# Kernel optimization log

Measured on AMD Instinct MI355X. Metric: run time of the kernel, lower is better.

Reference implementation:

```python
import jax, jax.numpy as jnp
import numpy as np

PATCH = 3  # match_patch_size

def _to_patches(fm, nph, npw):
    # fm: [1, C, H, W] -> [nph*npw, C*PATCH*PATCH] non-overlapping 3x3 patches
    C = fm.shape[1]
    x = fm[0, :, :nph * PATCH, :npw * PATCH].reshape(C, nph, PATCH, npw, PATCH)
    x = x.transpose(1, 3, 0, 2, 4)  # [nph, npw, C, p, p]
    return x.reshape(nph * npw, C * PATCH * PATCH)

def _from_patches(p, nph, npw, C):
    # [nph*npw, C*p*p] -> [1, C, nph*p, npw*p]
    x = p.reshape(nph, npw, C, PATCH, PATCH).transpose(2, 0, 3, 1, 4)
    return x.reshape(1, C, nph * PATCH, npw * PATCH)

def setup_inputs() -> dict:
    key = jax.random.key(0)
    k1, k2, k3 = jax.random.split(key, 3)
    C, H, W = 512, 252, 252
    style_fm = jax.random.normal(k1, (1, C, H, W), dtype=jnp.float32)
    img_fm = jax.random.normal(k2, (1, C, H, W), dtype=jnp.float32)
    mask = jax.random.uniform(k3, (1, 1, H, W), dtype=jnp.float32)
    return {"style_fm": style_fm, "img_fm": img_fm, "mask": mask}

def reference(style_fm, img_fm, mask):
    B, C, H, W = style_fm.shape  # B == 1
    nph, npw = H // PATCH, W // PATCH
    # Patch match: each img patch is a conv kernel applied to style_fm with
    # stride=PATCH -> score positions == non-overlapping style patch grid.
    img_p = _to_patches(img_fm, nph, npw)      # [P, D]
    sty_p = _to_patches(style_fm, nph, npw)    # [Q, D]
    scores = img_p @ sty_p.T                   # [P, Q] cross-correlation
    idx = jnp.argmax(scores, axis=1)           # best style patch per img patch
    matched = sty_p[idx]                       # [P, D] gather
    matched_fm = _from_patches(matched, nph, npw, C)
    style_matched = style_fm.at[:, :, :nph * PATCH, :npw * PATCH].set(matched_fm)
    # Mask (expanded as in capture_content), then Gram / sum(expanded mask)
    masked = style_matched * mask
    mask_sum = jnp.sum(jnp.broadcast_to(mask, style_matched.shape))
    gram = jnp.einsum('bchw,bdhw->bcd', masked, masked) / mask_sum  # [1, C, C]
    return gram
```

## Files before the change

### kernel.cpp

```cpp
#include <hip/hip_runtime.h>
#include <stdint.h>

typedef _Float16 f16;
typedef _Float16 f16x8 __attribute__((ext_vector_type(8)));
typedef float f32x4 __attribute__((ext_vector_type(4)));

#define NCH   512
#define IMH   252
#define IMW   252
#define HWSZ  (IMH*IMW)
#define NP    84
#define PN    (NP*NP)
#define PPAD  7168
#define DD    (NCH*9)
#define KK2   (PPAD*9)
#define KSPLIT 48
#define KCH   (KK2/KSPLIT)
#define MARGIN 1.0f

#define AS1(p) ((const __attribute__((address_space(1))) void*)(p))
#define AS3(p) ((__attribute__((address_space(3))) void*)(p))

__global__ void k_init(f16* __restrict__ I, f16* __restrict__ S,
                       int* cnt, float* msum) {
  unsigned t = blockIdx.x * blockDim.x + threadIdx.x;
  if (t == 0) { *cnt = 0; *msum = 0.0f; }
  const unsigned padN = (PPAD - PN) * DD;
  for (unsigned i = t; i < padN; i += gridDim.x * blockDim.x) {
    I[(size_t)PN * DD + i] = (f16)0.0f;
    S[(size_t)PN * DD + i] = (f16)0.0f;
  }
}

__global__ void k_masksum(const float* __restrict__ mask, float* msum) {
  __shared__ float red[256];
  float s = 0.f;
  for (unsigned i = blockIdx.x * 256 + threadIdx.x; i < HWSZ; i += gridDim.x * 256)
    s += mask[i];
  red[threadIdx.x] = s; __syncthreads();
  for (int st = 128; st > 0; st >>= 1) {
    if ((int)threadIdx.x < st) red[threadIdx.x] += red[threadIdx.x + st];
    __syncthreads();
  }
  if (threadIdx.x == 0) atomicAdd(msum, red[0]);
}

__global__ void k_pack(const float* __restrict__ fm, f16* __restrict__ out) {
  const unsigned total8 = PN * DD / 8;
  for (unsigned e8 = blockIdx.x * blockDim.x + threadIdx.x; e8 < total8;
       e8 += gridDim.x * blockDim.x) {
    const unsigned base = e8 * 8;
    const unsigned p = base / DD;
    const unsigned d0 = base - p * DD;
    const unsigned py = (p / NP) * 3, px = (p % NP) * 3;
    f16x8 v;
#pragma unroll
    for (int k = 0; k < 8; ++k) {
      unsigned d = d0 + k;
      unsigned c = d / 9, j = d - c * 9;
      v[k] = (f16)fm[(size_t)c * HWSZ + (py + j / 3) * IMW + px + j % 3];
    }
    *(f16x8*)(out + base) = v;
  }
}

__global__ __launch_bounds__(256, 3)
void k_gemm(const f16* __restrict__ A, const f16* __restrict__ B,
            f16* __restrict__ out) {
  __shared__ f16 As[128][32];
  __shared__ f16 Bs[128][32];
  const int tid = threadIdx.x;
  const int w = tid >> 6, l = tid & 63;
  const int nwg = (PPAD / 128) * (PPAD / 128);
  int bid = blockIdx.x;
  bid = (bid & 7) * (nwg >> 3) + (bid >> 3);
  const int bx = bid % (PPAD / 128), by = bid / (PPAD / 128);
  const size_t row0 = (size_t)by * 128, col0 = (size_t)bx * 128;
  const int wr = w >> 1, wc = w & 1;
  f32x4 acc[4][4] = {};
  const int sr = w * 32 + (l >> 2);
  const int skb = (l & 3) * 8;
  const f16* ga = A + (row0 + sr) * DD + skb;
  const f16* gb = B + (col0 + sr) * DD + skb;
  f16* lA0 = &As[w * 32][0];  f16* lA1 = &As[w * 32 + 16][0];
  f16* lB0 = &Bs[w * 32][0];  f16* lB1 = &Bs[w * 32 + 16][0];
  const int fr = l & 15, kb = (l >> 4) * 8;
  for (int k0 = 0; k0 < DD; k0 += 32) {
    __syncthreads();
    __builtin_amdgcn_global_load_lds(AS1(ga),           AS3(lA0), 16, 0, 0);
    __builtin_amdgcn_global_load_lds(AS1(ga + 16 * DD), AS3(lA1), 16, 0, 0);
    __builtin_amdgcn_global_load_lds(AS1(gb),           AS3(lB0), 16, 0, 0);
    __builtin_amdgcn_global_load_lds(AS1(gb + 16 * DD), AS3(lB1), 16, 0, 0);
    ga += 32; gb += 32;
    asm volatile("s_waitcnt vmcnt(0)" ::: "memory");
    __syncthreads();
    f16x8 af[4], bf[4];
#pragma unroll
    for (int i = 0; i < 4; ++i) af[i] = *(const f16x8*)&As[wr * 64 + i * 16 + fr][kb];
#pragma unroll
    for (int j = 0; j < 4; ++j) bf[j] = *(const f16x8*)&Bs[wc * 64 + j * 16 + fr][kb];
#pragma unroll
    for (int i = 0; i < 4; ++i)
#pragma unroll
      for (int j = 0; j < 4; ++j)
        acc[i][j] = __builtin_amdgcn_mfma_f32_16x16x32_f16(af[i], bf[j], acc[i][j], 0, 0, 0);
  }
  const int fq = l >> 4;
  const size_t orow = row0 + wr * 64, ocol = col0 + wc * 64;
#pragma unroll
  for (int i = 0; i < 4; ++i)
#pragma unroll
    for (int j = 0; j < 4; ++j)
#pragma unroll
      for (int r = 0; r < 4; ++r)
        out[(orow + i * 16 + fq * 4 + r) * PPAD + (ocol + j * 16 + fr)] =
            (f16)acc[i][j][r];
}

__global__ void k_top2(const f16* __restrict__ sc, int* __restrict__ idx,
                       float* __restrict__ max1v, int* __restrict__ amb, int* cnt) {
  const int p = blockIdx.x;
  const f16x8* row8 = (const f16x8*)(sc + (size_t)p * PPAD);
  float m1 = -1e30f, m2 = -1e30f; int i1 = 0;
  for (int v = threadIdx.x; v < PN / 8; v += 256) {
    f16x8 x = row8[v];
#pragma unroll
    for (int k = 0; k < 8; ++k) {
      float val = (float)x[k];
      if (val > m1) { m2 = m1; m1 = val; i1 = v * 8 + k; }
      else if (val > m2) m2 = val;
    }
  }
  __shared__ float sm1[256], sm2[256]; __shared__ int si1[256];
  const int t = threadIdx.x;
  sm1[t] = m1; sm2[t] = m2; si1[t] = i1; __syncthreads();
  for (int st = 128; st > 0; st >>= 1) {
    if (t < st) {
      float am1 = sm1[t], am2 = sm2[t]; int ai1 = si1[t];
      float bm1 = sm1[t + st], bm2 = sm2[t + st]; int bi1 = si1[t + st];
      if (bm1 > am1 || (bm1 == am1 && bi1 < ai1)) {
        sm1[t] = bm1; si1[t] = bi1; sm2[t] = fmaxf(am1, bm2);
      } else {
        sm2[t] = fmaxf(bm1, am2);
      }
    }
    __syncthreads();
  }
  if (t == 0) {
    idx[p] = si1[0]; max1v[p] = sm1[0];
    if (sm2[0] > sm1[0] - MARGIN) { int a = atomicAdd(cnt, 1); amb[a] = p; }
  }
}

__global__ void k_rescore(const float* __restrict__ img, const float* __restrict__ sty,
                          const f16* __restrict__ sc, const float* __restrict__ max1v,
                          const int* __restrict__ amb, const int* __restrict__ cnt,
                          int* __restrict__ idx) {
  __shared__ float red[256];
  __shared__ unsigned long long ball[4];
  const int t = threadIdx.x;
  const int n = *cnt;
  for (int r = blockIdx.x; r < n; r += gridDim.x) {
    const int p = amb[r];
    const float thr = max1v[p] - MARGIN;
    const f16* row = sc + (size_t)p * PPAD;
    const int py = (p / NP) * 3, px = (p % NP) * 3;
    float best = -1e30f; int bq = 0x7fffffff;
    for (int base = 0; base < PN; base += 256) {
      const int q = base + t;
      const bool is_cand = (q < PN) && ((float)row[q] >= thr);
      unsigned long long m = __ballot(is_cand);
      if ((t & 63) == 0) ball[t >> 6] = m;
      __syncthreads();
      for (int wv = 0; wv < 4; ++wv) {
        unsigned long long mm = ball[wv];
        while (mm) {
          const int b = __ffsll(mm) - 1; mm &= mm - 1;
          const int q2 = base + wv * 64 + b;
          const int qy = (q2 / NP) * 3, qx = (q2 % NP) * 3;
          float s = 0.f;
          for (int d = t; d < DD; d += 256) {
            int c = d / 9, j = d - c * 9, dy = j / 3, dx = j - dy * 3;
            s += img[(size_t)c * HWSZ + (py + dy) * IMW + (px + dx)] *
                 sty[(size_t)c * HWSZ + (qy + dy) * IMW + (qx + dx)];
          }
          red[t] = s; __syncthreads();
          for (int st = 128; st > 0; st >>= 1) {
            if (t < st) red[t] += red[t + st];
            __syncthreads();
          }
          const float tot = red[0];
          __syncthreads();
          if (tot > best || (tot == best && q2 < bq)) { best = tot; bq = q2; }
        }
      }
      __syncthreads();
    }
    if (t == 0) idx[p] = bq;
    __syncthreads();
  }
}

__global__ void k_masked(const f16* __restrict__ S, const int* __restrict__ idx,
                         const float* __restrict__ mask, f16* __restrict__ M) {
  const int p = blockIdx.x;
  if (p >= PN) {
    for (int e = threadIdx.x; e < NCH * 9; e += 256) {
      int c = e / 9, j = e - c * 9;
      M[(size_t)c * KK2 + p * 9 + j] = (f16)0.0f;
    }
    return;
  }
  __shared__ float mk[9];
  __shared__ int qs;
  if (threadIdx.x == 0) qs = idx[p];
  if (threadIdx.x < 9) {
    int j = threadIdx.x;
    mk[j] = mask[((p / NP) * 3 + j / 3) * IMW + (p % NP) * 3 + j % 3];
  }
  __syncthreads();
  const f16* srow = S + (size_t)qs * DD;
  for (int e = threadIdx.x; e < NCH * 9; e += 256) {
    int c = e / 9, j = e - c * 9;
    M[(size_t)c * KK2 + p * 9 + j] = (f16)((float)srow[e] * mk[j]);
  }
}

__global__ __launch_bounds__(256, 3)
void k_gram(const f16* __restrict__ M, float* __restrict__ part) {
  __shared__ f16 As[128][32];
  __shared__ f16 Bs[128][32];
  const int tid = threadIdx.x;
  const int w = tid >> 6, l = tid & 63;
  const int tile = blockIdx.x & 15, chunk = blockIdx.x >> 4;
  const int bx = tile & 3, by = tile >> 2;
  const size_t row0 = (size_t)by * 128, col0 = (size_t)bx * 128;
  const int wr = w >> 1, wc = w & 1;
  f32x4 acc[4][4] = {};
  const int sr = w * 32 + (l >> 2);
  const int skb = (l & 3) * 8;
  const int kbeg = chunk * KCH;
  const f16* ga = M + (row0 + sr) * KK2 + kbeg + skb;
  const f16* gb = M + (col0 + sr) * KK2 + kbeg + skb;
  f16* lA0 = &As[w * 32][0];  f16* lA1 = &As[w * 32 + 16][0];
  f16* lB0 = &Bs[w * 32][0];  f16* lB1 = &Bs[w * 32 + 16][0];
  const int fr = l & 15, kb = (l >> 4) * 8;
  for (int k0 = 0; k0 < KCH; k0 += 32) {
    __syncthreads();
    __builtin_amdgcn_global_load_lds(AS1(ga),            AS3(lA0), 16, 0, 0);
    __builtin_amdgcn_global_load_lds(AS1(ga + 16 * KK2), AS3(lA1), 16, 0, 0);
    __builtin_amdgcn_global_load_lds(AS1(gb),            AS3(lB0), 16, 0, 0);
    __builtin_amdgcn_global_load_lds(AS1(gb + 16 * KK2), AS3(lB1), 16, 0, 0);
    ga += 32; gb += 32;
    asm volatile("s_waitcnt vmcnt(0)" ::: "memory");
    __syncthreads();
    f16x8 af[4], bf[4];
#pragma unroll
    for (int i = 0; i < 4; ++i) af[i] = *(const f16x8*)&As[wr * 64 + i * 16 + fr][kb];
#pragma unroll
    for (int j = 0; j < 4; ++j) bf[j] = *(const f16x8*)&Bs[wc * 64 + j * 16 + fr][kb];
#pragma unroll
    for (int i = 0; i < 4; ++i)
#pragma unroll
      for (int j = 0; j < 4; ++j)
        acc[i][j] = __builtin_amdgcn_mfma_f32_16x16x32_f16(af[i], bf[j], acc[i][j], 0, 0, 0);
  }
  const int fq = l >> 4;
  const size_t orow = row0 + wr * 64, ocol = col0 + wc * 64;
  float* pout = part + (size_t)chunk * (NCH * NCH);
#pragma unroll
  for (int i = 0; i < 4; ++i)
#pragma unroll
    for (int j = 0; j < 4; ++j)
#pragma unroll
      for (int r = 0; r < 4; ++r)
        pout[(orow + i * 16 + fq * 4 + r) * NCH + (ocol + j * 16 + fr)] = acc[i][j][r];
}

__global__ void k_out(const float* __restrict__ part, const float* __restrict__ msum,
                      float* __restrict__ out) {
  const unsigned e = blockIdx.x * 256 + threadIdx.x;
  float s = 0.f;
#pragma unroll
  for (int k = 0; k < KSPLIT; ++k) s += part[(size_t)k * (NCH * NCH) + e];
  out[e] = s / (*msum * (float)NCH);
}

extern "C" void kernel_launch(void* const* d_in, const int* in_sizes, int n_in,
                              void* d_out, int out_size, void* d_ws, size_t ws_size,
                              hipStream_t stream) {
  const float* style = (const float*)d_in[0];
  const float* img   = (const float*)d_in[1];
  const float* mask  = (const float*)d_in[2];
  float* out = (float*)d_out;
  char* ws = (char*)d_ws;

  const size_t SZP = (size_t)PPAD * DD * sizeof(f16);
  const size_t SZS = (size_t)PPAD * PPAD * sizeof(f16);
  f16* I  = (f16*)(ws);
  f16* S  = (f16*)(ws + SZP);
  f16* SC = (f16*)(ws + 2 * SZP);
  char* misc = ws + 2 * SZP + SZS;
  int*   idx   = (int*)(misc);
  float* max1v = (float*)(misc + 32768);
  int*   amb   = (int*)(misc + 65536);
  int*   cnt   = (int*)(misc + 98304);
  float* msum  = (float*)(misc + 98432);
  float* part  = (float*)(ws);

  k_init   <<<256, 256, 0, stream>>>(I, S, cnt, msum);
  k_masksum<<<128, 256, 0, stream>>>(mask, msum);
  k_pack   <<<2048, 256, 0, stream>>>(img, I);
  k_pack   <<<2048, 256, 0, stream>>>(style, S);
  k_gemm   <<<(PPAD / 128) * (PPAD / 128), 256, 0, stream>>>(I, S, SC);
  k_top2   <<<PN, 256, 0, stream>>>(SC, idx, max1v, amb, cnt);
  k_rescore<<<512, 256, 0, stream>>>(img, style, SC, max1v, amb, cnt, idx);
  k_masked <<<PPAD, 256, 0, stream>>>(S, idx, mask, SC);
  k_gram   <<<16 * KSPLIT, 256, 0, stream>>>((const f16*)SC, part);
  k_out    <<<(NCH * NCH) / 256, 256, 0, stream>>>(part, msum, out);
}
```

Measured before the change: 1.421 ms.

## Use 256x256 pipelined GEMM and LDS-staged coalesced pack and masked-transpose kernels

Replaces the 128x128 score GEMM with a 512-thread 256x256 tile kernel that keeps a 4-deep LDS ring of async global-to-LDS loads, so memory latency overlaps with MFMA work and each loaded element is reused more. The patch-pack kernel now stages three image rows for 32 channels in LDS so global reads are coalesced, instead of issuing scattered per-element gathers. The masked-gather kernel likewise builds per-row tiles in LDS and writes the channel-major output contiguously, and zeroing of the padded region moves to a separate kernel. The larger tiles increase register and LDS use, which lowers occupancy and leaves fewer blocks to spread across the CUs.

```diff
diff --git a/kernel.cpp b/kernel.cpp
--- a/kernel.cpp
+++ b/kernel.cpp
@@ -45,70 +45,83 @@
   if (threadIdx.x == 0) atomicAdd(msum, red[0]);
 }
 
-__global__ void k_pack(const float* __restrict__ fm, f16* __restrict__ out) {
-  const unsigned total8 = PN * DD / 8;
-  for (unsigned e8 = blockIdx.x * blockDim.x + threadIdx.x; e8 < total8;
-       e8 += gridDim.x * blockDim.x) {
-    const unsigned base = e8 * 8;
-    const unsigned p = base / DD;
-    const unsigned d0 = base - p * DD;
-    const unsigned py = (p / NP) * 3, px = (p % NP) * 3;
-    f16x8 v;
+__global__ __launch_bounds__(256)
+void k_pack(const float* __restrict__ fm, f16* __restrict__ out) {
+  __shared__ f16 T[32 * 756];
+  const int py = blockIdx.x >> 4, cg = blockIdx.x & 15;
+  const int c0 = cg * 32;
+  for (int e = threadIdx.x; e < 32 * 756; e += 256) {
+    int cc = e / 756, rx = e - cc * 756;
+    T[e] = (f16)fm[(size_t)(c0 + cc) * HWSZ +
+                   (size_t)(py * 3 + rx / 252) * IMW + (rx % 252)];
+  }
+  __syncthreads();
+  for (int v = threadIdx.x; v < 84 * 36; v += 256) {
+    int pxi = v / 36, d0 = (v - pxi * 36) * 8;
+    f16x8 o;
 #pragma unroll
     for (int k = 0; k < 8; ++k) {
-      unsigned d = d0 + k;
-      unsigned c = d / 9, j = d - c * 9;
-      v[k] = (f16)fm[(size_t)c * HWSZ + (py + j / 3) * IMW + px + j % 3];
-    }
-    *(f16x8*)(out + base) = v;
-  }
-}
-
-__global__ __launch_bounds__(256, 3)
-void k_gemm(const f16* __restrict__ A, const f16* __restrict__ B,
-            f16* __restrict__ out) {
-  __shared__ f16 As[128][32];
-  __shared__ f16 Bs[128][32];
-  const int tid = threadIdx.x;
-  const int w = tid >> 6, l = tid & 63;
-  const int nwg = (PPAD / 128) * (PPAD / 128);
+      int d = d0 + k, cc = d / 9, j = d - cc * 9;
+      o[k] = T[cc * 756 + (j / 3) * 252 + pxi * 3 + (j % 3)];
+    }
+    *(f16x8*)(out + (size_t)(py * NP + pxi) * DD + c0 * 9 + d0) = o;
+  }
+}
+
+__global__ __launch_bounds__(512, 2)
+void k_gemm256(const f16* __restrict__ A, const f16* __restrict__ B,
+               f16* __restrict__ out) {
+  __shared__ f16 Al[4][256][32];
+  __shared__ f16 Bl[4][256][32];
+  const int tid = threadIdx.x, w = tid >> 6, l = tid & 63;
   int bid = blockIdx.x;
-  bid = (bid & 7) * (nwg >> 3) + (bid >> 3);
-  const int bx = bid % (PPAD / 128), by = bid / (PPAD / 128);
-  const size_t row0 = (size_t)by * 128, col0 = (size_t)bx * 128;
-  const int wr = w >> 1, wc = w & 1;
-  f32x4 acc[4][4] = {};
-  const int sr = w * 32 + (l >> 2);
-  const int skb = (l & 3) * 8;
-  const f16* ga = A + (row0 + sr) * DD + skb;
-  const f16* gb = B + (col0 + sr) * DD + skb;
-  f16* lA0 = &As[w * 32][0];  f16* lA1 = &As[w * 32 + 16][0];
-  f16* lB0 = &Bs[w * 32][0];  f16* lB1 = &Bs[w * 32 + 16][0];
+  bid = (bid & 7) * 98 + (bid >> 3);
+  const int bx = bid % 28, by = bid / 28;
+  const size_t row0 = (size_t)by * 256, col0 = (size_t)bx * 256;
+  const int wm = w >> 2, wn = w & 3;
+  f32x4 acc[8][4] = {};
+  const int srow = w * 16 + (l >> 2);
+  const int scol = (l & 3) * 8;
+  const f16* gA0 = A + (row0 + srow) * DD + scol;
+  const f16* gA1 = A + (row0 + srow + 128) * DD + scol;
+  const f16* gB0 = B + (col0 + srow) * DD + scol;
+  const f16* gB1 = B + (col0 + srow + 128) * DD + scol;
+  const int ldst = w * 512 + l * 8;
+#define STG(tt, bb) do {                                                        \
+    __builtin_amdgcn_global_load_lds(AS1(gA0 + (tt)*32), AS3(&Al[bb][0][0] + ldst),        16, 0, 0); \
+    __builtin_amdgcn_global_load_lds(AS1(gA1 + (tt)*32), AS3(&Al[bb][0][0] + 4096 + ldst), 16, 0, 0); \
+    __builtin_amdgcn_global_load_lds(AS1(gB0 + (tt)*32), AS3(&Bl[bb][0][0] + ldst),        16, 0, 0); \
+    __builtin_amdgcn_global_load_lds(AS1(gB1 + (tt)*32), AS3(&Bl[bb][0][0] + 4096 + ldst), 16, 0, 0); \
+  } while (0)
+  STG(0, 0); STG(1, 1); STG(2, 2);
   const int fr = l & 15, kb = (l >> 4) * 8;
-  for (int k0 = 0; k0 < DD; k0 += 32) {
-    __syncthreads();
-    __builtin_amdgcn_global_load_lds(AS1(ga),           AS3(lA0), 16, 0, 0);
-    __builtin_amdgcn_global_load_lds(AS1(ga + 16 * DD), AS3(lA1), 16, 0, 0);
-    __builtin_amdgcn_global_load_lds(AS1(gb),           AS3(lB0), 16, 0, 0);
-    __builtin_amdgcn_global_load_lds(AS1(gb + 16 * DD), AS3(lB1), 16, 0, 0);
-    ga += 32; gb += 32;
-    asm volatile("s_waitcnt vmcnt(0)" ::: "memory");
-    __syncthreads();
-    f16x8 af[4], bf[4];
-#pragma unroll
-    for (int i = 0; i < 4; ++i) af[i] = *(const f16x8*)&As[wr * 64 + i * 16 + fr][kb];
-#pragma unroll
-    for (int j = 0; j < 4; ++j) bf[j] = *(const f16x8*)&Bs[wc * 64 + j * 16 + fr][kb];
-#pragma unroll
-    for (int i = 0; i < 4; ++i)
+  const int NT = DD / 32;
+  for (int t = 0; t < NT; ++t) {
+    const int ts = (t + 3 < NT) ? t + 3 : NT - 1;
+    const int bb = t & 3;
+    STG(ts, (t + 3) & 3);
+    asm volatile("s_waitcnt vmcnt(12)" ::: "memory");
+    __builtin_amdgcn_s_barrier();
+    __builtin_amdgcn_sched_barrier(0);
+    f16x8 af[8], bf[4];
+#pragma unroll
+    for (int i = 0; i < 8; ++i) af[i] = *(const f16x8*)&Al[bb][wm * 128 + i * 16 + fr][kb];
+#pragma unroll
+    for (int j = 0; j < 4; ++j) bf[j] = *(const f16x8*)&Bl[bb][wn * 64 + j * 16 + fr][kb];
+#pragma unroll
+    for (int i = 0; i < 8; ++i)
 #pragma unroll
       for (int j = 0; j < 4; ++j)
         acc[i][j] = __builtin_amdgcn_mfma_f32_16x16x32_f16(af[i], bf[j], acc[i][j], 0, 0, 0);
-  }
+    asm volatile("s_waitcnt lgkmcnt(0)" ::: "memory");
+    __builtin_amdgcn_sched_barrier(0);
+    __builtin_amdgcn_s_barrier();
+  }
+#undef STG
   const int fq = l >> 4;
-  const size_t orow = row0 + wr * 64, ocol = col0 + wc * 64;
-#pragma unroll
-  for (int i = 0; i < 4; ++i)
+  const size_t orow = row0 + wm * 128, ocol = col0 + wn * 64;
+#pragma unroll
+  for (int i = 0; i < 8; ++i)
 #pragma unroll
     for (int j = 0; j < 4; ++j)
 #pragma unroll
@@ -201,28 +214,44 @@
   }
 }
 
-__global__ void k_masked(const f16* __restrict__ S, const int* __restrict__ idx,
-                         const float* __restrict__ mask, f16* __restrict__ M) {
-  const int p = blockIdx.x;
-  if (p >= PN) {
-    for (int e = threadIdx.x; e < NCH * 9; e += 256) {
-      int c = e / 9, j = e - c * 9;
-      M[(size_t)c * KK2 + p * 9 + j] = (f16)0.0f;
-    }
-    return;
-  }
-  __shared__ float mk[9];
-  __shared__ int qs;
-  if (threadIdx.x == 0) qs = idx[p];
-  if (threadIdx.x < 9) {
-    int j = threadIdx.x;
-    mk[j] = mask[((p / NP) * 3 + j / 3) * IMW + (p % NP) * 3 + j % 3];
-  }
+__global__ __launch_bounds__(256)
+void k_masked(const f16* __restrict__ S, const int* __restrict__ idx,
+              const float* __restrict__ mask, f16* __restrict__ M) {
+  __shared__ f16 B[84 * 288];
+  __shared__ float mrow[756];
+  __shared__ int qv[84];
+  const int py = blockIdx.x >> 4, cg = blockIdx.x & 15;
+  const int c0 = cg * 32;
+  for (int e = threadIdx.x; e < 756; e += 256)
+    mrow[e] = mask[(size_t)(py * 3 + e / 252) * IMW + (e % 252)];
+  if (threadIdx.x < 84) qv[threadIdx.x] = idx[py * NP + threadIdx.x];
   __syncthreads();
-  const f16* srow = S + (size_t)qs * DD;
-  for (int e = threadIdx.x; e < NCH * 9; e += 256) {
-    int c = e / 9, j = e - c * 9;
-    M[(size_t)c * KK2 + p * 9 + j] = (f16)((float)srow[e] * mk[j]);
+  for (int v = threadIdx.x; v < 84 * 36; v += 256) {
+    int pxi = v / 36, d0 = (v - pxi * 36) * 8;
+    f16x8 x = *(const f16x8*)(S + (size_t)qv[pxi] * DD + c0 * 9 + d0);
+    f16x8 o;
+#pragma unroll
+    for (int k = 0; k < 8; ++k) {
+      int j = (d0 + k) % 9;
+      o[k] = (f16)((float)x[k] * mrow[(j / 3) * 252 + pxi * 3 + (j % 3)]);
+    }
+    *(f16x8*)(&B[pxi * 288 + d0]) = o;
+  }
+  __syncthreads();
+  for (int e = threadIdx.x; e < 32 * 756; e += 256) {
+    int cc = e / 756, r = e - cc * 756;
+    M[(size_t)(c0 + cc) * KK2 + (size_t)py * 756 + r] =
+        B[(r / 9) * 288 + cc * 9 + (r % 9)];
+  }
+}
+
+__global__ void k_mpad(f16* __restrict__ M) {
+  const unsigned per_c = (PPAD - PN) * 9;
+  const unsigned total = NCH * per_c;
+  for (unsigned e = blockIdx.x * 256 + threadIdx.x; e < total;
+       e += gridDim.x * 256) {
+    unsigned c = e / per_c, r = e - c * per_c;
+    M[(size_t)c * KK2 + (size_t)PN * 9 + r] = (f16)0.0f;
   }
 }
 
@@ -310,12 +339,13 @@
 
   k_init   <<<256, 256, 0, stream>>>(I, S, cnt, msum);
   k_masksum<<<128, 256, 0, stream>>>(mask, msum);
-  k_pack   <<<2048, 256, 0, stream>>>(img, I);
-  k_pack   <<<2048, 256, 0, stream>>>(style, S);
-  k_gemm   <<<(PPAD / 128) * (PPAD / 128), 256, 0, stream>>>(I, S, SC);
+  k_pack   <<<84 * 16, 256, 0, stream>>>(img, I);
+  k_pack   <<<84 * 16, 256, 0, stream>>>(style, S);
+  k_gemm256<<<(PPAD / 256) * (PPAD / 256), 512, 0, stream>>>(I, S, SC);
   k_top2   <<<PN, 256, 0, stream>>>(SC, idx, max1v, amb, cnt);
   k_rescore<<<512, 256, 0, stream>>>(img, style, SC, max1v, amb, cnt, idx);
-  k_masked <<<PPAD, 256, 0, stream>>>(S, idx, mask, SC);
+  k_masked <<<84 * 16, 256, 0, stream>>>(S, idx, mask, SC);
+  k_mpad   <<<128, 256, 0, stream>>>(SC);
   k_gram   <<<16 * KSPLIT, 256, 0, stream>>>((const f16*)SC, part);
   k_out    <<<(NCH * NCH) / 256, 256, 0, stream>>>(part, msum, out);
 }
```

Result: faster. 1.316 ms (-7.4%).
